# Kernel tuning notes

Hardware: AMD Instinct MI355X
Metric: run time of the kernel (lower is better)

## Reference

```python
import jax, jax.numpy as jnp
import numpy as np

EMB = 1024
HEADS = 16
HEAD_DIM = EMB // HEADS
EPS = 1e-5


def gelu_tanh(x):
    c = jnp.sqrt(jnp.asarray(2.0 / jnp.pi, x.dtype))
    return 0.5 * x * (1.0 + jnp.tanh(c * (x + 0.044715 * x ** 3)))


def layernorm(x, scale, shift):
    mean = jnp.mean(x, axis=-1, keepdims=True)
    var = jnp.mean((x - mean) ** 2, axis=-1, keepdims=True)  # unbiased=False
    return scale * (x - mean) / jnp.sqrt(var + EPS) + shift


def setup_inputs() -> dict:
    key = jax.random.key(0)
    ks = jax.random.split(key, 12)
    d, dff = EMB, 4 * EMB
    sd = 1.0 / np.sqrt(d)
    inp = {
        "x": jax.random.normal(ks[0], (2, 2048, d), jnp.float32),
        "Wq": jax.random.normal(ks[1], (d, d), jnp.float32) * sd,
        "Wk": jax.random.normal(ks[2], (d, d), jnp.float32) * sd,
        "Wv": jax.random.normal(ks[3], (d, d), jnp.float32) * sd,
        "Wo": jax.random.normal(ks[4], (d, d), jnp.float32) * sd,
        "bo": jnp.zeros((d,), jnp.float32),
        "W1": jax.random.normal(ks[5], (d, dff), jnp.float32) * sd,
        "b1": jnp.zeros((dff,), jnp.float32),
        "W2": jax.random.normal(ks[6], (dff, d), jnp.float32) * (1.0 / np.sqrt(dff)),
        "b2": jnp.zeros((d,), jnp.float32),
        "g1": jnp.ones((d,), jnp.float32),
        "s1": jnp.zeros((d,), jnp.float32),
        "g2": jnp.ones((d,), jnp.float32),
        "s2": jnp.zeros((d,), jnp.float32),
    }
    return inp


def attention(x, Wq, Wk, Wv, Wo, bo):
    b, s, d = x.shape
    def heads(W):
        return (x @ W).reshape(b, s, HEADS, HEAD_DIM).transpose(0, 2, 1, 3)  # b h s hd
    q, k, v = heads(Wq), heads(Wk), heads(Wv)
    scores = jnp.einsum("bhqd,bhkd->bhqk", q, k)
    causal = jnp.tril(jnp.ones((s, s), bool))
    scores = jnp.where(causal, scores, -jnp.inf)
    w = jax.nn.softmax(scores / np.sqrt(HEAD_DIM), axis=-1)
    ctx = jnp.einsum("bhqk,bhkd->bqhd", w, v).reshape(b, s, d)
    return ctx @ Wo + bo


def reference(x, Wq, Wk, Wv, Wo, bo, W1, b1, W2, b2, g1, s1, g2, s2):
    h = x + attention(layernorm(x, g1, s1), Wq, Wk, Wv, Wo, bo)
    y = layernorm(h, g2, s2)
    y = gelu_tanh(y @ W1 + b1) @ W2 + b2
    return h + y
```

## Files before the change

### kernel.cpp

```cpp
#include <hip/hip_runtime.h>
#include <hip/hip_bf16.h>
#include <stdint.h>
#include <math.h>

#define EMB   1024
#define DFF   4096
#define HEADS 16
#define HD    64
#define BATCH 2
#define SEQ   2048
#define ROWS  (BATCH * SEQ)

typedef __hip_bfloat16 bf16;
typedef short bf16x8_t __attribute__((ext_vector_type(8)));
typedef float f32x4_t __attribute__((ext_vector_type(4)));

typedef const uint32_t __attribute__((address_space(1)))* gp_t;
typedef uint32_t __attribute__((address_space(3)))* lp_t;

__device__ __forceinline__ void async_copy16(const bf16* g, short* l) {
    __builtin_amdgcn_global_load_lds((gp_t)(const void*)g, (lp_t)(void*)l, 16, 0, 0);
}

__device__ __forceinline__ void wait_lds() {
    __asm__ volatile("" ::: "memory");
    __builtin_amdgcn_s_waitcnt(0xC07F);
    __asm__ volatile("" ::: "memory");
}

__device__ __forceinline__ float gelu_f(float x) {
    float z = 0.7978845608028654f * (x + 0.044715f * x * x * x);
    float e = __builtin_amdgcn_exp2f(z * 2.885390081777927f);
    float t = 1.0f - 2.0f * __builtin_amdgcn_rcpf(e + 1.0f);
    return 0.5f * x * (1.0f + t);
}

__device__ __forceinline__ short bf16_bits(float x) {
    bf16 b = (bf16)x;
    short s;
    __builtin_memcpy(&s, &b, 2);
    return s;
}

__device__ __forceinline__ bf16x8_t load8(const bf16* p) {
    bf16x8_t v;
    __builtin_memcpy(&v, p, 16);
    return v;
}

template<int EPI, int BM>
__global__ __launch_bounds__(256) void gemm_k(
    const bf16* __restrict__ A, const bf16* __restrict__ BT,
    bf16* __restrict__ outB, float* __restrict__ outF,
    const float* __restrict__ bias, const float* __restrict__ resF,
    int N, int K, size_t bStrideZ, size_t cStrideZ)
{
    __shared__ alignas(16) short As[2][BM * 32];
    __shared__ alignas(16) short Bs[2][128 * 32];
    constexpr int AI  = BM / 32;
    constexpr int AIS = BM / 64;
    const int tid  = threadIdx.x;
    const int wave = tid >> 6;
    const int lane = tid & 63;
    const int quad = lane >> 4;
    const int l16  = lane & 15;
    const int m0 = blockIdx.y * BM;
    const int n0 = blockIdx.x * 128;
    const int wm = (wave >> 1) * (BM / 2);
    const int wn = (wave & 1) * 64;

    const bf16* Bz = BT + (size_t)blockIdx.z * bStrideZ;

    const bf16* Ag[AIS]; int aoff[AIS];
    const bf16* Bg[2];   int boff[2];
    #pragma unroll
    for (int i = 0; i < AIS; i++) {
        const int c = i * 256 + tid;
        const int row = c >> 2;
        const int lch = (c & 3) ^ ((row >> 1) & 3);
        Ag[i]   = A + (size_t)(m0 + row) * K + lch * 8;
        aoff[i] = (i * 256 + wave * 64) * 8;
    }
    #pragma unroll
    for (int i = 0; i < 2; i++) {
        const int c = i * 256 + tid;
        const int row = c >> 2;
        const int lch = (c & 3) ^ ((row >> 1) & 3);
        Bg[i]   = Bz + (size_t)(n0 + row) * K + lch * 8;
        boff[i] = (i * 256 + wave * 64) * 8;
    }

    f32x4_t acc[AI][4] = {};

    #pragma unroll
    for (int i = 0; i < AIS; i++) async_copy16(Ag[i], &As[0][aoff[i]]);
    #pragma unroll
    for (int i = 0; i < 2; i++)   async_copy16(Bg[i], &Bs[0][boff[i]]);
    __syncthreads();

    int cur = 0;
    for (int k0 = 0; k0 < K; k0 += 32) {
        const int kn = k0 + 32;
        if (kn < K) {
            #pragma unroll
            for (int i = 0; i < AIS; i++) async_copy16(Ag[i] + kn, &As[cur ^ 1][aoff[i]]);
            #pragma unroll
            for (int i = 0; i < 2; i++)   async_copy16(Bg[i] + kn, &Bs[cur ^ 1][boff[i]]);
        }
        bf16x8_t a[AI], b[4];
        #pragma unroll
        for (int i = 0; i < AI; i++) {
            const int r = wm + i * 16 + l16;
            a[i] = *(const bf16x8_t*)&As[cur][r * 32 + ((quad ^ ((r >> 1) & 3)) << 3)];
        }
        #pragma unroll
        for (int j = 0; j < 4; j++) {
            const int r = wn + j * 16 + l16;
            b[j] = *(const bf16x8_t*)&Bs[cur][r * 32 + ((quad ^ ((r >> 1) & 3)) << 3)];
        }
        #pragma unroll
        for (int i = 0; i < AI; i++)
            #pragma unroll
            for (int j = 0; j < 4; j++)
                acc[i][j] = __builtin_amdgcn_mfma_f32_16x16x32_bf16(
                    a[i], b[j], acc[i][j], 0, 0, 0);
        __syncthreads();
        cur ^= 1;
    }

    bf16* outBz = (EPI == 0) ? outB + (size_t)blockIdx.z * cStrideZ : outB;
    #pragma unroll
    for (int j = 0; j < 4; j++) {
        const int col = n0 + wn + j * 16 + l16;
        float bv = 0.0f;
        if constexpr (EPI != 0) bv = bias[col];
        #pragma unroll
        for (int i = 0; i < AI; i++) {
            #pragma unroll
            for (int r = 0; r < 4; r++) {
                const int row = m0 + wm + i * 16 + quad * 4 + r;
                float v = acc[i][j][r] + bv;
                if constexpr (EPI == 1 || EPI == 3) {
                    v += resF[(size_t)row * N + col];
                    outF[(size_t)row * N + col] = v;
                } else if constexpr (EPI == 2) {
                    outBz[(size_t)row * N + col] = (bf16)gelu_f(v);
                } else {
                    outBz[(size_t)row * N + col] = (bf16)v;
                }
            }
        }
    }
}

__global__ __launch_bounds__(256) void ln_k(
    const float* __restrict__ x, const float* __restrict__ g,
    const float* __restrict__ s, bf16* __restrict__ out)
{
    const int row = blockIdx.x;
    const int t = threadIdx.x;
    const size_t base = (size_t)row * EMB + t * 4;
    float v[4];
    #pragma unroll
    for (int e = 0; e < 4; e++) v[e] = x[base + e];
    float sum = v[0] + v[1] + v[2] + v[3];
    float sq  = v[0]*v[0] + v[1]*v[1] + v[2]*v[2] + v[3]*v[3];
    #pragma unroll
    for (int o = 1; o < 64; o <<= 1) {
        sum += __shfl_xor(sum, o);
        sq  += __shfl_xor(sq, o);
    }
    __shared__ float ssum[4], ssq[4];
    const int wave = t >> 6;
    if ((t & 63) == 0) { ssum[wave] = sum; ssq[wave] = sq; }
    __syncthreads();
    sum = ssum[0] + ssum[1] + ssum[2] + ssum[3];
    sq  = ssq[0] + ssq[1] + ssq[2] + ssq[3];
    const float mean = sum * (1.0f / EMB);
    const float var  = sq * (1.0f / EMB) - mean * mean;
    const float rstd = rsqrtf(var + 1e-5f);
    #pragma unroll
    for (int e = 0; e < 4; e++)
        out[base + e] = (bf16)(g[t * 4 + e] * (v[e] - mean) * rstd + s[t * 4 + e]);
}

template<typename T>
__global__ __launch_bounds__(256) void transpose_k(
    const T* __restrict__ src, bf16* __restrict__ dst, int R, int C)
{
    __shared__ bf16 tile[64][65];
    const size_t bo = (size_t)blockIdx.z * R * C;
    const int tx = threadIdx.x, ty = threadIdx.y;
    const int r0 = blockIdx.y * 64, c0 = blockIdx.x * 64;
    #pragma unroll
    for (int i = 0; i < 16; i++) {
        int r = ty + i * 4;
        tile[r][tx] = (bf16)(float)src[bo + (size_t)(r0 + r) * C + c0 + tx];
    }
    __syncthreads();
    #pragma unroll
    for (int i = 0; i < 16; i++) {
        int c = ty + i * 4;
        dst[bo + (size_t)(c0 + c) * R + r0 + tx] = tile[tx][c];
    }
}

__global__ __launch_bounds__(256) void transpose3_k(
    const float* __restrict__ s0, const float* __restrict__ s1,
    const float* __restrict__ s2, bf16* __restrict__ dst, int R, int C)
{
    __shared__ bf16 tile[64][65];
    const float* src = blockIdx.z == 0 ? s0 : (blockIdx.z == 1 ? s1 : s2);
    bf16* d = dst + (size_t)blockIdx.z * R * C;
    const int tx = threadIdx.x, ty = threadIdx.y;
    const int r0 = blockIdx.y * 64, c0 = blockIdx.x * 64;
    #pragma unroll
    for (int i = 0; i < 16; i++) {
        int r = ty + i * 4;
        tile[r][tx] = (bf16)src[(size_t)(r0 + r) * C + c0 + tx];
    }
    __syncthreads();
    #pragma unroll
    for (int i = 0; i < 16; i++) {
        int c = ty + i * 4;
        d[(size_t)(c0 + c) * R + r0 + tx] = tile[tx][c];
    }
}

__global__ __launch_bounds__(256) void attn_k(
    const bf16* __restrict__ q, const bf16* __restrict__ k,
    const bf16* __restrict__ vt, bf16* __restrict__ ctx)
{
    __shared__ alignas(16) short Ks[2][64 * 64];
    __shared__ alignas(16) short Vs[2][64 * 64];
    __shared__ alignas(16) short P[4][16 * 40];
    const int tid = threadIdx.x;
    const int wv = tid >> 6;
    const int lane = tid & 63;
    const int quad = lane >> 4, l16 = lane & 15;

    const int fid = (int)blockIdx.x;
    const int lid = (fid & 7) * 128 + (fid >> 3);
    const int chunk = 31 - (lid & 31);
    const int h = (lid >> 5) & 15;
    const int b = lid >> 9;
    const size_t rowBase = (size_t)b * SEQ;
    const int qb = chunk * 64 + wv * 16;
    const int NK = chunk + 1;

    const bf16* kcol  = k + rowBase * EMB + h * HD;
    const bf16* vbase = vt + (size_t)(b * HEADS + h) * HD * SEQ;

    bf16x8_t aq[2];
    #pragma unroll
    for (int s2 = 0; s2 < 2; s2++)
        aq[s2] = load8(&q[(rowBase + qb + l16) * EMB + h * HD + s2 * 32 + quad * 8]);

    f32x4_t O[4] = {};
    float l_p[4] = {};

    int krw[2], kgc[2];
    #pragma unroll
    for (int i = 0; i < 2; i++) {
        const int c = i * 256 + tid;
        krw[i] = c >> 3;
        kgc[i] = (c & 7) ^ (krw[i] & 7);
    }
    const int ldsOff[2] = { (0 * 256 + wv * 64) * 8, (1 * 256 + wv * 64) * 8 };

    #pragma unroll
    for (int i = 0; i < 2; i++) {
        async_copy16(kcol + (size_t)krw[i] * EMB + kgc[i] * 8, &Ks[0][ldsOff[i]]);
        async_copy16(vbase + (size_t)krw[i] * SEQ + kgc[i] * 8, &Vs[0][ldsOff[i]]);
    }
    __syncthreads();

    constexpr float SC = 0.125f * 1.44269504088896f;

    int cur = 0;
    for (int kb = 0; kb < NK; ++kb) {
        const int kbase = kb * 64;
        if (kb + 1 < NK) {
            const int nb = kbase + 64;
            #pragma unroll
            for (int i = 0; i < 2; i++) {
                async_copy16(kcol + (size_t)(nb + krw[i]) * EMB + kgc[i] * 8,
                             &Ks[cur ^ 1][ldsOff[i]]);
                async_copy16(vbase + (size_t)krw[i] * SEQ + nb + kgc[i] * 8,
                             &Vs[cur ^ 1][ldsOff[i]]);
            }
        }
        bf16x8_t ck[4][2];
        #pragma unroll
        for (int nt = 0; nt < 4; nt++) {
            const int kr = nt * 16 + l16;
            #pragma unroll
            for (int s2 = 0; s2 < 2; s2++)
                ck[nt][s2] = *(const bf16x8_t*)
                    &Ks[cur][kr * 64 + (((s2 * 4 + quad) ^ (kr & 7)) << 3)];
        }
        f32x4_t sc[4] = {};
        #pragma unroll
        for (int nt = 0; nt < 4; nt++)
            #pragma unroll
            for (int s2 = 0; s2 < 2; s2++)
                sc[nt] = __builtin_amdgcn_mfma_f32_16x16x32_bf16(
                    aq[s2], ck[nt][s2], sc[nt], 0, 0, 0);

        short* Pw = P[wv];
        const bool full = (kbase + 63 <= qb);
        #pragma unroll
        for (int hf = 0; hf < 2; hf++) {
            bf16x8_t cv[4];
            #pragma unroll
            for (int c = 0; c < 4; c++) {
                const int vr = c * 16 + l16;
                cv[c] = *(const bf16x8_t*)
                    &Vs[cur][vr * 64 + (((hf * 4 + quad) ^ (vr & 7)) << 3)];
            }
            if (full) {
                #pragma unroll
                for (int nt2 = 0; nt2 < 2; nt2++) {
                    const int nt = hf * 2 + nt2;
                    #pragma unroll
                    for (int r = 0; r < 4; r++) {
                        const float p = __builtin_amdgcn_exp2f(sc[nt][r] * SC);
                        l_p[r] += p;
                        Pw[(quad * 4 + r) * 40 + nt2 * 16 + l16] = bf16_bits(p);
                    }
                }
            } else {
                #pragma unroll
                for (int nt2 = 0; nt2 < 2; nt2++) {
                    const int nt = hf * 2 + nt2;
                    const int kk = kbase + nt * 16 + l16;
                    #pragma unroll
                    for (int r = 0; r < 4; r++) {
                        const int qg = qb + quad * 4 + r;
                        float s = sc[nt][r] * SC;
                        if (kk > qg) s = -1e30f;
                        const float p = __builtin_amdgcn_exp2f(s);
                        l_p[r] += p;
                        Pw[(quad * 4 + r) * 40 + nt2 * 16 + l16] = bf16_bits(p);
                    }
                }
            }
            wait_lds();
            bf16x8_t pa = *(const bf16x8_t*)&Pw[l16 * 40 + quad * 8];
            #pragma unroll
            for (int c = 0; c < 4; c++)
                O[c] = __builtin_amdgcn_mfma_f32_16x16x32_bf16(pa, cv[c], O[c], 0, 0, 0);
        }
        __syncthreads();
        cur ^= 1;
    }

    #pragma unroll
    for (int r = 0; r < 4; r++) {
        float l = l_p[r];
        l += __shfl_xor(l, 1);
        l += __shfl_xor(l, 2);
        l += __shfl_xor(l, 4);
        l += __shfl_xor(l, 8);
        const float inv = 1.0f / l;
        #pragma unroll
        for (int c = 0; c < 4; c++)
            ctx[(rowBase + qb + quad * 4 + r) * EMB + h * HD + c * 16 + l16]
                = (bf16)(O[c][r] * inv);
    }
}

extern "C" void kernel_launch(void* const* d_in, const int* in_sizes, int n_in,
                              void* d_out, int out_size, void* d_ws, size_t ws_size,
                              hipStream_t stream) {
    const float* X  = (const float*)d_in[0];
    const float* Wq = (const float*)d_in[1];
    const float* Wk = (const float*)d_in[2];
    const float* Wv = (const float*)d_in[3];
    const float* Wo = (const float*)d_in[4];
    const float* bo = (const float*)d_in[5];
    const float* W1 = (const float*)d_in[6];
    const float* b1 = (const float*)d_in[7];
    const float* W2 = (const float*)d_in[8];
    const float* b2 = (const float*)d_in[9];
    const float* g1 = (const float*)d_in[10];
    const float* s1 = (const float*)d_in[11];
    const float* g2 = (const float*)d_in[12];
    const float* s2 = (const float*)d_in[13];
    float* out = (float*)d_out;

    char* ws = (char*)d_ws;
    const size_t MB = 1024 * 1024;
    bf16*  lnbuf = (bf16*)(ws + 0);
    bf16*  qkv   = (bf16*)(ws + 8 * MB);
    bf16*  vtb   = (bf16*)(ws + 32 * MB);
    bf16*  ctx   = (bf16*)(ws + 40 * MB);
    float* hbuf  = (float*)(ws + 48 * MB);
    bf16*  WqT   = (bf16*)(ws + 64 * MB);
    bf16*  WoT   = (bf16*)(ws + 70 * MB);
    bf16*  ffn1  = (bf16*)(ws + 8 * MB);
    bf16*  W1T   = (bf16*)(ws + 40 * MB);
    bf16*  W2T   = (bf16*)(ws + 64 * MB);

    const dim3 tb(64, 4);
    transpose3_k<<<dim3(16, 16, 3), tb, 0, stream>>>(Wq, Wk, Wv, WqT, EMB, EMB);
    transpose_k<float><<<dim3(16, 16, 1), tb, 0, stream>>>(Wo, WoT, EMB, EMB);

    ln_k<<<ROWS, 256, 0, stream>>>(X, g1, s1, lnbuf);

    gemm_k<0, 128><<<dim3(8, 32, 3), 256, 0, stream>>>(
        lnbuf, WqT, qkv, nullptr, nullptr, nullptr,
        EMB, EMB, (size_t)EMB * EMB, (size_t)ROWS * EMB);

    transpose_k<bf16><<<dim3(16, 32, BATCH), tb, 0, stream>>>(
        qkv + (size_t)2 * ROWS * EMB, vtb, SEQ, EMB);

    attn_k<<<1024, 256, 0, stream>>>(
        qkv, qkv + (size_t)ROWS * EMB, vtb, ctx);

    gemm_k<1, 64><<<dim3(8, 64), 256, 0, stream>>>(
        ctx, WoT, nullptr, hbuf, bo, X, EMB, EMB, 0, 0);

    transpose_k<float><<<dim3(64, 16, 1), tb, 0, stream>>>(W1, W1T, EMB, DFF);
    transpose_k<float><<<dim3(16, 64, 1), tb, 0, stream>>>(W2, W2T, DFF, EMB);

    ln_k<<<ROWS, 256, 0, stream>>>(hbuf, g2, s2, lnbuf);

    gemm_k<2, 128><<<dim3(32, 32), 256, 0, stream>>>(
        lnbuf, W1T, ffn1, nullptr, b1, nullptr, DFF, EMB, 0, 0);

    gemm_k<3, 64><<<dim3(8, 64), 256, 0, stream>>>(
        ffn1, W2T, nullptr, out, b2, hbuf, EMB, DFF, 0, 0);
}
```

Baseline: 380.2 us.

## Triple-buffer GEMM LDS tiles with partial vmcnt waits for deeper prefetch

Moves the GEMM mainloop from double to triple buffering in LDS, so loads run two K-steps ahead. The full __syncthreads is replaced by an s_waitcnt that waits only for the older load group (vmcnt=NV) before the barrier. This keeps more global loads in flight and hides memory latency. In exchange it uses 50% more LDS, which may reduce occupancy, and it depends on the vmcnt encoding and load counts being exactly right.

```diff
diff --git a/kernel.cpp b/kernel.cpp
--- a/kernel.cpp
+++ b/kernel.cpp
@@ -55,10 +55,11 @@
     const float* __restrict__ bias, const float* __restrict__ resF,
     int N, int K, size_t bStrideZ, size_t cStrideZ)
 {
-    __shared__ alignas(16) short As[2][BM * 32];
-    __shared__ alignas(16) short Bs[2][128 * 32];
+    __shared__ alignas(16) short As[3][BM * 32];
+    __shared__ alignas(16) short Bs[3][128 * 32];
     constexpr int AI  = BM / 32;
     constexpr int AIS = BM / 64;
+    constexpr int NV  = AIS + 2;
     const int tid  = threadIdx.x;
     const int wave = tid >> 6;
     const int lane = tid & 63;
@@ -92,31 +93,44 @@
 
     f32x4_t acc[AI][4] = {};
 
+    const int T = K >> 5;
+
     #pragma unroll
     for (int i = 0; i < AIS; i++) async_copy16(Ag[i], &As[0][aoff[i]]);
     #pragma unroll
     for (int i = 0; i < 2; i++)   async_copy16(Bg[i], &Bs[0][boff[i]]);
-    __syncthreads();
-
-    int cur = 0;
-    for (int k0 = 0; k0 < K; k0 += 32) {
-        const int kn = k0 + 32;
-        if (kn < K) {
-            #pragma unroll
-            for (int i = 0; i < AIS; i++) async_copy16(Ag[i] + kn, &As[cur ^ 1][aoff[i]]);
-            #pragma unroll
-            for (int i = 0; i < 2; i++)   async_copy16(Bg[i] + kn, &Bs[cur ^ 1][boff[i]]);
+    #pragma unroll
+    for (int i = 0; i < AIS; i++) async_copy16(Ag[i] + 32, &As[1][aoff[i]]);
+    #pragma unroll
+    for (int i = 0; i < 2; i++)   async_copy16(Bg[i] + 32, &Bs[1][boff[i]]);
+
+    __asm__ volatile("" ::: "memory");
+    __builtin_amdgcn_s_waitcnt(0x0F70 | NV);
+    __builtin_amdgcn_sched_barrier(0);
+    __builtin_amdgcn_s_barrier();
+    __builtin_amdgcn_sched_barrier(0);
+    __asm__ volatile("" ::: "memory");
+
+    int cb = 0;
+    for (int t = 0; t < T; ++t) {
+        if (t + 2 < T) {
+            const int sb = (cb == 0) ? 2 : cb - 1;
+            const int k0 = (t + 2) * 32;
+            #pragma unroll
+            for (int i = 0; i < AIS; i++) async_copy16(Ag[i] + k0, &As[sb][aoff[i]]);
+            #pragma unroll
+            for (int i = 0; i < 2; i++)   async_copy16(Bg[i] + k0, &Bs[sb][boff[i]]);
         }
         bf16x8_t a[AI], b[4];
         #pragma unroll
         for (int i = 0; i < AI; i++) {
             const int r = wm + i * 16 + l16;
-            a[i] = *(const bf16x8_t*)&As[cur][r * 32 + ((quad ^ ((r >> 1) & 3)) << 3)];
+            a[i] = *(const bf16x8_t*)&As[cb][r * 32 + ((quad ^ ((r >> 1) & 3)) << 3)];
         }
         #pragma unroll
         for (int j = 0; j < 4; j++) {
             const int r = wn + j * 16 + l16;
-            b[j] = *(const bf16x8_t*)&Bs[cur][r * 32 + ((quad ^ ((r >> 1) & 3)) << 3)];
+            b[j] = *(const bf16x8_t*)&Bs[cb][r * 32 + ((quad ^ ((r >> 1) & 3)) << 3)];
         }
         #pragma unroll
         for (int i = 0; i < AI; i++)
@@ -124,8 +138,17 @@
             for (int j = 0; j < 4; j++)
                 acc[i][j] = __builtin_amdgcn_mfma_f32_16x16x32_bf16(
                     a[i], b[j], acc[i][j], 0, 0, 0);
-        __syncthreads();
-        cur ^= 1;
+
+        if (t + 1 < T) {
+            __asm__ volatile("" ::: "memory");
+            if (t + 2 < T) __builtin_amdgcn_s_waitcnt(0x0F70 | NV);
+            else           __builtin_amdgcn_s_waitcnt(0x0F70);
+            __builtin_amdgcn_sched_barrier(0);
+            __builtin_amdgcn_s_barrier();
+            __builtin_amdgcn_sched_barrier(0);
+            __asm__ volatile("" ::: "memory");
+        }
+        cb = (cb == 2) ? 0 : cb + 1;
     }
 
     bf16* outBz = (EPI == 0) ? outB + (size_t)blockIdx.z * cStrideZ : outB;
```

New measurement: 391.9 us. 1.03x slower.
